# Optimization experiments

Measured on AMD Instinct MI355X. Metric: run time of the kernel, lower is better.

Reference implementation:

```python
import jax, jax.numpy as jnp
import numpy as np

N, C_IN, C_OUT, H, RANK = 16, 4, 32, 400, 4


def setup_inputs() -> dict:
    key = jax.random.key(0)
    k1, k2, k3 = jax.random.split(key, 3)
    x = jax.random.normal(k1, (N, C_IN, H, H), dtype=jnp.float32)
    # symmetric sylo: weight_R tied to weight_L (shape C_out x C_in x H x rank)
    fan_in = C_IN * H
    scale = 1.0 / np.sqrt(fan_in)
    weight_L = jax.random.normal(k2, (C_OUT, C_IN, H, RANK), dtype=jnp.float32) * scale
    bias = jax.random.uniform(k3, (C_OUT,), dtype=jnp.float32, minval=-scale, maxval=scale)
    return {"x": x, "weight_L": weight_L, "bias": bias}


def reference(x, weight_L, bias):
    # Expand low-rank symmetric template: T[o,c] = L[o,c] @ L[o,c].T  (H x H)
    T = jnp.einsum('ocir,ocjr->ocij', weight_L, weight_L)
    # Crosshair similarity, summed over input channels:
    # out[n,o,i,j] = sum_c [ sum_k X[n,c,i,k]T[o,c,i,k] + sum_k X[n,c,k,j]T[o,c,k,j] - X[n,c,i,j]T[o,c,i,j] ]
    rows = jnp.einsum('ncik,ocik->noi', x, T)   # row sums of X*T
    cols = jnp.einsum('nckj,ockj->noj', x, T)   # column sums of X*T
    diag = jnp.einsum('ncij,ocij->noij', x, T)  # pointwise term (counted twice)
    out = rows[..., :, None] + cols[..., None, :] - diag
    return out + bias[None, :, None, None]
```

## Files before the change

### kernel.cpp

```cpp
#include <hip/hip_runtime.h>

#define H  400
#define NB 16
#define CI 4
#define CO 32

#define TT 80
__global__ __launch_bounds__(256) void k_transpose(const float* __restrict__ x,
                                                   float* __restrict__ xt) {
    __shared__ float tile[TT][TT + 5];
    int b = blockIdx.x;
    int tj = b % 5;
    int ti = (b / 5) % 5;
    int nc = b / 25;
    const float* src = x + (size_t)nc * H * H;
    float* dst = xt + (size_t)nc * H * H;
    int i0 = ti * TT, j0 = tj * TT;
    for (int e = threadIdx.x; e < TT * 20; e += 256) {
        int r = e / 20, q = e % 20;
        float4 v = ((const float4*)(src + (size_t)(i0 + r) * H + j0))[q];
        tile[r][q * 4 + 0] = v.x; tile[r][q * 4 + 1] = v.y;
        tile[r][q * 4 + 2] = v.z; tile[r][q * 4 + 3] = v.w;
    }
    __syncthreads();
    for (int e = threadIdx.x; e < TT * 20; e += 256) {
        int r = e / 20, q = e % 20;
        float4 v;
        v.x = tile[q * 4 + 0][r]; v.y = tile[q * 4 + 1][r];
        v.z = tile[q * 4 + 2][r]; v.w = tile[q * 4 + 3][r];
        ((float4*)(dst + (size_t)(j0 + r) * H + i0))[q] = v;
    }
}

#define KC 40
#define KSPLIT 5
__global__ __launch_bounds__(256) void k_rowscols(const float* __restrict__ x,
        const float* __restrict__ xt, const float* __restrict__ L,
        float* __restrict__ rowsP, float* __restrict__ colsP)
{
    __shared__ __align__(16) float4 Lm[CO * CI];
    __shared__ __align__(16) float Xr[NB * CI * KC];
    __shared__ __align__(16) float Xc[NB * CI * KC];
    __shared__ __align__(16) float Tr[CO * 164];
    int b = blockIdx.x;
    int m  = b / KSPLIT;
    int ks = b % KSPLIT;
    int tid = threadIdx.x;
    const float4* L4 = (const float4*)L;
    if (tid < CO * CI) Lm[tid] = L4[tid * H + m];

    int o  = tid & 31;
    int n0 = tid >> 5;
    int n1 = n0 + 8;
    float ar0 = 0.f, ar1 = 0.f, ac0 = 0.f, ac1 = 0.f;

    for (int ch = 0; ch < 2; ++ch) {
        int k0 = ks * 80 + ch * KC;
        __syncthreads();
        for (int e = tid; e < NB * CI * KC / 4; e += 256) {
            int q  = e % 10;
            int nc = e / 10;
            ((float4*)Xr)[e] = *(const float4*)(x  + (size_t)(nc * H + m) * H + k0 + q * 4);
            ((float4*)Xc)[e] = *(const float4*)(xt + (size_t)(nc * H + m) * H + k0 + q * 4);
        }
        for (int e = tid; e < CO * CI * KC; e += 256) {
            int k  = e % KC;
            int oc = e / KC;
            float4 lv = L4[oc * H + k0 + k];
            float4 lm = Lm[oc];
            Tr[(oc >> 2) * 164 + (oc & 3) * KC + k] =
                lv.x * lm.x + lv.y * lm.y + lv.z * lm.z + lv.w * lm.w;
        }
        __syncthreads();
        #pragma unroll
        for (int c = 0; c < CI; ++c) {
            const float4* trp = (const float4*)(Tr + o * 164 + c * KC);
            const float4* pr0 = (const float4*)(Xr + (n0 * CI + c) * KC);
            const float4* pr1 = (const float4*)(Xr + (n1 * CI + c) * KC);
            const float4* pc0 = (const float4*)(Xc + (n0 * CI + c) * KC);
            const float4* pc1 = (const float4*)(Xc + (n1 * CI + c) * KC);
            #pragma unroll
            for (int q = 0; q < KC / 4; ++q) {
                float4 tv = trp[q];
                float4 a  = pr0[q];
                float4 bb = pr1[q];
                float4 cc = pc0[q];
                float4 dd = pc1[q];
                ar0 += tv.x * a.x  + tv.y * a.y  + tv.z * a.z  + tv.w * a.w;
                ar1 += tv.x * bb.x + tv.y * bb.y + tv.z * bb.z + tv.w * bb.w;
                ac0 += tv.x * cc.x + tv.y * cc.y + tv.z * cc.z + tv.w * cc.w;
                ac1 += tv.x * dd.x + tv.y * dd.y + tv.z * dd.z + tv.w * dd.w;
            }
        }
    }
    size_t base = (size_t)ks * NB * CO * H;
    rowsP[base + (size_t)(n0 * CO + o) * H + m] = ar0;
    rowsP[base + (size_t)(n1 * CO + o) * H + m] = ar1;
    colsP[base + (size_t)(n0 * CO + o) * H + m] = ac0;
    colsP[base + (size_t)(n1 * CO + o) * H + m] = ac1;
}

__global__ __launch_bounds__(256) void k_reduce(const float* __restrict__ rowsP,
        const float* __restrict__ colsP, float* __restrict__ rows, float* __restrict__ cols)
{
    int i = blockIdx.x * 256 + threadIdx.x;
    if (i < NB * CO * H) {
        float s = 0.f, t = 0.f;
        #pragma unroll
        for (int k = 0; k < KSPLIT; ++k) {
            s += rowsP[(size_t)k * NB * CO * H + i];
            t += colsP[(size_t)k * NB * CO * H + i];
        }
        rows[i] = s;
        cols[i] = t;
    }
}

#define TS 16
__global__ __launch_bounds__(512) void k_out(const float* __restrict__ x,
        const float* __restrict__ L, const float* __restrict__ bias,
        const float* __restrict__ rows, const float* __restrict__ cols,
        float* __restrict__ out)
{
    __shared__ __align__(16) float Xl[NB * CI * TS * TS];
    __shared__ __align__(16) float rT[NB * 8 * TS];
    __shared__ __align__(16) float cT[NB * 8 * TS];
    int b = blockIdx.x;
    int ti = b / 25, tj = b % 25;
    int i0 = ti * TS, j0 = tj * TS;
    int tid = threadIdx.x;

    const float4* x4 = (const float4*)x;
    float4* Xl4 = (float4*)Xl;
    for (int e = tid; e < NB * CI * TS * 4; e += 512) {
        int q  = e & 3;
        int ii = (e >> 2) & 15;
        int nc = e >> 6;
        Xl4[e] = x4[(size_t)(nc * H + i0 + ii) * 100 + tj * 4 + q];
    }

    int o  = tid >> 6;
    int u  = tid & 63;
    int ii = u >> 2, jq = u & 3;
    const float4* L4 = (const float4*)L;
    const float4* cT4 = (const float4*)cT;
    float4* out4 = (float4*)out;

    for (int os = 0; os < 4; ++os) {
        int og = os * 8 + o;
        float4 T4[CI];
        #pragma unroll
        for (int c = 0; c < CI; ++c) {
            float4 Li = L4[(og * CI + c) * H + i0 + ii];
            float4 La = L4[(og * CI + c) * H + j0 + jq * 4 + 0];
            float4 Lb = L4[(og * CI + c) * H + j0 + jq * 4 + 1];
            float4 Lc = L4[(og * CI + c) * H + j0 + jq * 4 + 2];
            float4 Ld = L4[(og * CI + c) * H + j0 + jq * 4 + 3];
            T4[c].x = Li.x * La.x + Li.y * La.y + Li.z * La.z + Li.w * La.w;
            T4[c].y = Li.x * Lb.x + Li.y * Lb.y + Li.z * Lb.z + Li.w * Lb.w;
            T4[c].z = Li.x * Lc.x + Li.y * Lc.y + Li.z * Lc.z + Li.w * Lc.w;
            T4[c].w = Li.x * Ld.x + Li.y * Ld.y + Li.z * Ld.z + Li.w * Ld.w;
        }
        float bo = bias[og];

        __syncthreads();
        for (int e = tid; e < NB * 8 * TS; e += 512) {
            int iw = e & 15;
            int oo = (e >> 4) & 7;
            int n  = e >> 7;
            rT[e] = rows[(size_t)(n * CO + os * 8 + oo) * H + i0 + iw];
            cT[e] = cols[(size_t)(n * CO + os * 8 + oo) * H + j0 + iw];
        }
        __syncthreads();

        for (int n = 0; n < NB; ++n) {
            float ra = rT[(n * 8 + o) * TS + ii] + bo;
            float4 ca = cT4[(n * 8 + o) * 4 + jq];
            float4 acc;
            acc.x = ra + ca.x; acc.y = ra + ca.y; acc.z = ra + ca.z; acc.w = ra + ca.w;
            #pragma unroll
            for (int c = 0; c < CI; ++c) {
                float4 xv = Xl4[((n * CI + c) * TS + ii) * 4 + jq];
                acc.x -= xv.x * T4[c].x;
                acc.y -= xv.y * T4[c].y;
                acc.z -= xv.z * T4[c].z;
                acc.w -= xv.w * T4[c].w;
            }
            out4[((size_t)(n * CO + og) * H + i0 + ii) * 100 + tj * 4 + jq] = acc;
        }
    }
}

extern "C" void kernel_launch(void* const* d_in, const int* in_sizes, int n_in,
                              void* d_out, int out_size, void* d_ws, size_t ws_size,
                              hipStream_t stream) {
    const float* x    = (const float*)d_in[0];
    const float* L    = (const float*)d_in[1];
    const float* bias = (const float*)d_in[2];
    float* out = (float*)d_out;
    char* ws = (char*)d_ws;

    size_t xt_bytes = (size_t)NB * CI * H * H * sizeof(float);
    size_t rc_elems = (size_t)NB * CO * H;
    size_t rcP_bytes = (size_t)KSPLIT * rc_elems * sizeof(float);
    size_t rc_bytes  = rc_elems * sizeof(float);

    float* XT    = (float*)ws;
    float* rowsP = (float*)(ws + xt_bytes);
    float* colsP = (float*)(ws + xt_bytes + rcP_bytes);
    float* rows  = (float*)(ws + xt_bytes + 2 * rcP_bytes);
    float* cols  = (float*)(ws + xt_bytes + 2 * rcP_bytes + rc_bytes);
    (void)ws_size;

    k_transpose<<<1600, 256, 0, stream>>>(x, XT);
    k_rowscols<<<H * KSPLIT, 256, 0, stream>>>(x, XT, L, rowsP, colsP);
    k_reduce<<<(NB * CO * H + 255) / 256, 256, 0, stream>>>(rowsP, colsP, rows, cols);
    k_out<<<625, 512, 0, stream>>>(x, L, bias, rows, cols, out);
}
```

Before: 509.2 us.

## Retile output kernel to 8x32 tiles split over batch quarters

The output kernel now tiles each block as 8 rows by 32 columns and covers only 4 batch items, launching 2600 blocks instead of 625. Each output row segment becomes 128 bytes wide instead of 64, which should coalesce the dominant output writes better, and the extra blocks improve occupancy and load balance. In exchange, the low-rank template product is recomputed for each batch quarter. The last column tile is shifted to overlap its neighbour, so some output elements are written twice.

```diff
diff --git a/kernel.cpp b/kernel.cpp
--- a/kernel.cpp
+++ b/kernel.cpp
@@ -116,33 +116,41 @@
     }
 }
 
-#define TS 16
+#define OI 8
+#define OJ 32
 __global__ __launch_bounds__(512) void k_out(const float* __restrict__ x,
         const float* __restrict__ L, const float* __restrict__ bias,
         const float* __restrict__ rows, const float* __restrict__ cols,
         float* __restrict__ out)
 {
-    __shared__ __align__(16) float Xl[NB * CI * TS * TS];
-    __shared__ __align__(16) float rT[NB * 8 * TS];
-    __shared__ __align__(16) float cT[NB * 8 * TS];
-    int b = blockIdx.x;
-    int ti = b / 25, tj = b % 25;
-    int i0 = ti * TS, j0 = tj * TS;
+    __shared__ __align__(16) float Xl[16 * OI * OJ];
+    __shared__ __align__(16) float rT[4 * 8 * OI];
+    __shared__ __align__(16) float cT[4 * 8 * OJ];
+    int b  = blockIdx.x;
+    int nq = b / 650;
+    int r2 = b % 650;
+    int ib = r2 / 13, jb = r2 % 13;
+    int i0 = ib * OI;
+    int j0 = (jb < 12) ? jb * OJ : (H - OJ);
+    int n0 = nq * 4;
     int tid = threadIdx.x;
 
     const float4* x4 = (const float4*)x;
     float4* Xl4 = (float4*)Xl;
-    for (int e = tid; e < NB * CI * TS * 4; e += 512) {
-        int q  = e & 3;
-        int ii = (e >> 2) & 15;
-        int nc = e >> 6;
-        Xl4[e] = x4[(size_t)(nc * H + i0 + ii) * 100 + tj * 4 + q];
-    }
-
-    int o  = tid >> 6;
-    int u  = tid & 63;
-    int ii = u >> 2, jq = u & 3;
-    const float4* L4 = (const float4*)L;
+    for (int e = tid; e < 1024; e += 512) {
+        int q  = e & 7;
+        int i  = (e >> 3) & 7;
+        int pl = e >> 6;
+        Xl4[e] = x4[(size_t)(n0 * 4 + pl) * (H * 100) + (size_t)(i0 + i) * 100 + (j0 >> 2) + q];
+    }
+
+    int o    = tid >> 6;
+    int lane = tid & 63;
+    int i    = lane >> 3;
+    int jq   = lane & 7;
+    int gi   = i0 + i;
+    int gj4  = (j0 >> 2) + jq;
+    const float4* L4  = (const float4*)L;
     const float4* cT4 = (const float4*)cT;
     float4* out4 = (float4*)out;
 
@@ -151,7 +159,7 @@
         float4 T4[CI];
         #pragma unroll
         for (int c = 0; c < CI; ++c) {
-            float4 Li = L4[(og * CI + c) * H + i0 + ii];
+            float4 Li = L4[(og * CI + c) * H + gi];
             float4 La = L4[(og * CI + c) * H + j0 + jq * 4 + 0];
             float4 Lb = L4[(og * CI + c) * H + j0 + jq * 4 + 1];
             float4 Lc = L4[(og * CI + c) * H + j0 + jq * 4 + 2];
@@ -164,29 +172,31 @@
         float bo = bias[og];
 
         __syncthreads();
-        for (int e = tid; e < NB * 8 * TS; e += 512) {
-            int iw = e & 15;
-            int oo = (e >> 4) & 7;
-            int n  = e >> 7;
-            rT[e] = rows[(size_t)(n * CO + os * 8 + oo) * H + i0 + iw];
-            cT[e] = cols[(size_t)(n * CO + os * 8 + oo) * H + j0 + iw];
-        }
-        __syncthreads();
-
-        for (int n = 0; n < NB; ++n) {
-            float ra = rT[(n * 8 + o) * TS + ii] + bo;
-            float4 ca = cT4[(n * 8 + o) * 4 + jq];
+        if (tid < 256) {
+            int ii = tid & 7, oo = (tid >> 3) & 7, nl = tid >> 6;
+            rT[tid] = rows[(size_t)((n0 + nl) * CO + os * 8 + oo) * H + i0 + ii];
+        }
+        for (int e = tid; e < 1024; e += 512) {
+            int jj = e & 31, oo = (e >> 5) & 7, nl = e >> 8;
+            cT[e] = cols[(size_t)((n0 + nl) * CO + os * 8 + oo) * H + j0 + jj];
+        }
+        __syncthreads();
+
+        #pragma unroll
+        for (int nl = 0; nl < 4; ++nl) {
+            float ra = rT[(nl * 8 + o) * OI + i] + bo;
+            float4 ca = cT4[(nl * 8 + o) * (OJ / 4) + jq];
             float4 acc;
             acc.x = ra + ca.x; acc.y = ra + ca.y; acc.z = ra + ca.z; acc.w = ra + ca.w;
             #pragma unroll
             for (int c = 0; c < CI; ++c) {
-                float4 xv = Xl4[((n * CI + c) * TS + ii) * 4 + jq];
+                float4 xv = Xl4[((nl * 4 + c) * OI + i) * (OJ / 4) + jq];
                 acc.x -= xv.x * T4[c].x;
                 acc.y -= xv.y * T4[c].y;
                 acc.z -= xv.z * T4[c].z;
                 acc.w -= xv.w * T4[c].w;
             }
-            out4[((size_t)(n * CO + og) * H + i0 + ii) * 100 + tj * 4 + jq] = acc;
+            out4[(size_t)((n0 + nl) * CO + og) * (H * 100) + (size_t)gi * 100 + gj4] = acc;
         }
     }
 }
@@ -215,5 +225,5 @@
     k_transpose<<<1600, 256, 0, stream>>>(x, XT);
     k_rowscols<<<H * KSPLIT, 256, 0, stream>>>(x, XT, L, rowsP, colsP);
     k_reduce<<<(NB * CO * H + 255) / 256, 256, 0, stream>>>(rowsP, colsP, rows, cols);
-    k_out<<<625, 512, 0, stream>>>(x, L, bias, rows, cols, out);
-}
+    k_out<<<2600, 512, 0, stream>>>(x, L, bias, rows, cols, out);
+}
```

Measured after the change: 536.4 us. 5.3% more time.
